# Kernel tuning notes

Measured on AMD Instinct MI355X. Metric: run time of the kernel, lower is better.

The kernel has to match this reference:

```python
import jax, jax.numpy as jnp
import numpy as np

B, C, H, W = 8, 320, 64, 64
NUM_SAMPLES = 3


def _skew(v):
    z = jnp.zeros((), v.dtype)
    return jnp.stack([
        jnp.stack([z, -v[2], v[1]]),
        jnp.stack([v[2], z, -v[0]]),
        jnp.stack([-v[1], v[0], z]),
    ])


def _rodrigues(rv):
    theta = jnp.linalg.norm(rv)
    r = rv / jnp.maximum(theta, 1e-12)
    I = jnp.eye(3, dtype=rv.dtype)
    R = jnp.cos(theta) * I + (1 - jnp.cos(theta)) * jnp.outer(r, r) + jnp.sin(theta) * _skew(r)
    return jnp.where(theta < 1e-6, I, R)


def _fundamental(Ks, Kt, ps, pt):
    Rs = jax.vmap(_rodrigues)(ps[:, :3])
    Rt = jax.vmap(_rodrigues)(pt[:, :3])
    ts, tt = ps[:, 3:], pt[:, 3:]
    R_rel = jnp.einsum('bij,bkj->bik', Rs, Rt)          # R_s @ R_t^T
    t_rel = ts - jnp.einsum('bij,bj->bi', R_rel, tt)
    E = jnp.einsum('bij,bjk->bik', jax.vmap(_skew)(t_rel), R_rel)
    inv_Ks = jnp.linalg.inv(Ks)
    inv_Kt = jnp.linalg.inv(Kt)
    return jnp.einsum('bji,bjk,bkl->bil', inv_Kt, E, inv_Ks)  # inv(Kt)^T @ E @ inv(Ks)


def _epipolar_warp(x, Ks, Kt, ps, pt, conv_w, conv_b):
    Bs, Cc, Hh, Ww = x.shape
    Fm = _fundamental(Ks, Kt, ps, pt)
    # pixel homogeneous coords, row-major flatten; H==W makes torch's i*H+j
    # loop index identical to this flat order
    k = jnp.arange(Hh * Ww)
    px = (k % Ww).astype(x.dtype)
    py = (k // Ww).astype(x.dtype)
    P = jnp.stack([px, py, jnp.ones_like(px)])            # [3, HW]
    lines = jnp.einsum('bji,jn->bin', Fm, P)              # F^T @ P -> [B,3,HW]
    a, b, c = lines[:, 0], lines[:, 1], lines[:, 2]
    W1, H1 = float(Ww - 1), float(Hh - 1)
    EPS = 1e-10
    x1 = jnp.clip(-c / (a + EPS), 0.0, W1)
    x2 = jnp.clip(-(b * H1 + c) / (a + EPS), 0.0, W1)
    y1 = jnp.clip(-c / (b + EPS), 0.0, H1)
    y2 = jnp.clip(-(a * W1 + c) / (b + EPS), 0.0, H1)
    t = jnp.linspace(0.0, 1.0, NUM_SAMPLES, dtype=x.dtype)
    sx = (x1[..., None] * (1 - t) + x2[..., None] * t).reshape(Bs, -1)  # [B, HW*3]
    sy = (y1[..., None] * (1 - t) + y2[..., None] * t).reshape(Bs, -1)
    # bilinear sampling; grid_sample(align_corners=True) normalization round-trips
    # back to pixel coords, and all samples are in-bounds by construction
    x0 = jnp.floor(sx)
    y0 = jnp.floor(sy)
    wx = sx - x0
    wy = sy - y0
    x0i = jnp.clip(x0, 0, Ww - 1).astype(jnp.int32)
    x1i = jnp.clip(x0 + 1, 0, Ww - 1).astype(jnp.int32)
    y0i = jnp.clip(y0, 0, Hh - 1).astype(jnp.int32)
    y1i = jnp.clip(y0 + 1, 0, Hh - 1).astype(jnp.int32)
    flat = x.reshape(Bs, Cc, Hh * Ww)

    def gather(yi, xi):
        return jnp.take_along_axis(flat, (yi * Ww + xi)[:, None, :], axis=2)  # [B,C,HW*3]

    g00, g10 = gather(y0i, x0i), gather(y0i, x1i)
    g01, g11 = gather(y1i, x0i), gather(y1i, x1i)
    wx_, wy_ = wx[:, None], wy[:, None]
    val = (g00 * (1 - wx_) * (1 - wy_) + g10 * wx_ * (1 - wy_)
           + g01 * (1 - wx_) * wy_ + g11 * wx_ * wy_)
    sampled = val.reshape(Bs, Cc, Hh * Ww, NUM_SAMPLES).mean(-1).reshape(Bs, Cc, Hh, Ww)
    out = jax.lax.conv_general_dilated(sampled, conv_w, (1, 1), 'SAME',
                                       dimension_numbers=('NCHW', 'OIHW', 'NCHW'))
    out = out + conv_b[None, :, None, None]
    return jax.nn.relu(out)


def setup_inputs() -> dict:
    key = jax.random.key(0)
    ks = jax.random.split(key, 8)
    x = jax.random.normal(ks[0], (B, C, H, W), dtype=jnp.float32)

    def make_K(kk):
        f = jax.random.uniform(kk, (B,), minval=400.0, maxval=600.0, dtype=jnp.float32)
        K = jnp.zeros((B, 3, 3), jnp.float32)
        K = K.at[:, 0, 0].set(f).at[:, 1, 1].set(f)
        K = K.at[:, 0, 2].set(W / 2.0).at[:, 1, 2].set(H / 2.0).at[:, 2, 2].set(1.0)
        return K

    source_intrinsics = make_K(ks[1])
    target_intrinsics = make_K(ks[2])
    source_pose = jnp.concatenate([
        0.3 * jax.random.normal(ks[3], (B, 3), jnp.float32),
        jax.random.normal(ks[4], (B, 3), jnp.float32)], axis=1)
    target_pose = jnp.concatenate([
        0.3 * jax.random.normal(ks[5], (B, 3), jnp.float32),
        jax.random.normal(ks[6], (B, 3), jnp.float32)], axis=1)
    fan_in = C * 3 * 3
    conv_w = jax.random.normal(ks[7], (C, C, 3, 3), jnp.float32) / np.sqrt(fan_in)
    conv_b = jnp.zeros((C,), jnp.float32)
    return {"x": x, "source_intrinsics": source_intrinsics,
            "target_intrinsics": target_intrinsics, "source_pose": source_pose,
            "target_pose": target_pose, "conv_w": conv_w, "conv_b": conv_b}


def reference(x, source_intrinsics, target_intrinsics, source_pose, target_pose, conv_w, conv_b):
    return _epipolar_warp(x, source_intrinsics, target_intrinsics,
                          source_pose, target_pose, conv_w, conv_b)
```

## Files before the change

### kernel.cpp

```cpp
#include <hip/hip_runtime.h>
#include <math.h>

#define BATCH 8
#define CH 320
#define HW 4096

typedef unsigned short u16;
typedef __attribute__((ext_vector_type(8))) short bf16x8;
typedef __attribute__((ext_vector_type(8))) unsigned short u16x8;
typedef __attribute__((ext_vector_type(4))) float f32x4;
typedef __attribute__((ext_vector_type(4))) float float4v;

#define ZP_OFF 0
#define SAMP_OFF 788480
#define WT_OFF 21760000

#define IBUF_BYTES 17408
#define A_OFF (2*IBUF_BYTES)
#define APHASE 61440
#define LDS_TOTAL (A_OFF + 2*APHASE)

__device__ __forceinline__ u16 f2bf(float f) {
    union { float f; unsigned u; } v; v.f = f;
    unsigned r = v.u + 0x7fffu + ((v.u >> 16) & 1u);
    return (u16)(r >> 16);
}
__device__ __forceinline__ float bf2f(u16 h) {
    union { unsigned u; float f; } v; v.u = ((unsigned)h) << 16;
    return v.f;
}
__device__ __forceinline__ void gl_lds16(const void* g, void* l) {
    __builtin_amdgcn_global_load_lds(
        (const __attribute__((address_space(1))) unsigned*)g,
        (__attribute__((address_space(3))) unsigned*)l, 16, 0, 0);
}

__device__ __forceinline__ void rodrigues3(float rv0, float rv1, float rv2, float* R) {
    float theta = sqrtf(rv0*rv0 + rv1*rv1 + rv2*rv2);
    float it = 1.0f / fmaxf(theta, 1e-12f);
    float r0 = rv0*it, r1 = rv1*it, r2 = rv2*it;
    float c = cosf(theta), s = sinf(theta), o = 1.0f - c;
    R[0]=c+o*r0*r0;    R[1]=o*r0*r1-s*r2; R[2]=o*r0*r2+s*r1;
    R[3]=o*r1*r0+s*r2; R[4]=c+o*r1*r1;    R[5]=o*r1*r2-s*r0;
    R[6]=o*r2*r0-s*r1; R[7]=o*r2*r1+s*r0; R[8]=c+o*r2*r2;
    if (theta < 1e-6f) { R[0]=1;R[1]=0;R[2]=0;R[3]=0;R[4]=1;R[5]=0;R[6]=0;R[7]=0;R[8]=1; }
}

__device__ __forceinline__ void inv3(const float* M, float* o) {
    float a=M[0],b=M[1],c=M[2],d=M[3],e=M[4],f=M[5],g=M[6],h=M[7],i=M[8];
    float A = e*i - f*h, B = f*g - d*i, C = d*h - e*g;
    float id = 1.0f / (a*A + b*B + c*C);
    o[0]=A*id;         o[1]=(c*h-b*i)*id; o[2]=(b*f-c*e)*id;
    o[3]=B*id;         o[4]=(a*i-c*g)*id; o[5]=(c*d-a*f)*id;
    o[6]=C*id;         o[7]=(b*g-a*h)*id; o[8]=(a*e-b*d)*id;
}

__device__ void compute_F(const float* Ks, const float* Kt, const float* ps,
                          const float* pt, int b, float* Fm) {
    float Rs[9], Rt[9];
    rodrigues3(ps[b*6+0], ps[b*6+1], ps[b*6+2], Rs);
    rodrigues3(pt[b*6+0], pt[b*6+1], pt[b*6+2], Rt);
    float Rr[9];
    #pragma unroll
    for (int i = 0; i < 3; ++i)
      #pragma unroll
      for (int k = 0; k < 3; ++k)
        Rr[i*3+k] = Rs[i*3+0]*Rt[k*3+0] + Rs[i*3+1]*Rt[k*3+1] + Rs[i*3+2]*Rt[k*3+2];
    float tt0 = pt[b*6+3], tt1 = pt[b*6+4], tt2 = pt[b*6+5];
    float tr0 = ps[b*6+3] - (Rr[0]*tt0 + Rr[1]*tt1 + Rr[2]*tt2);
    float tr1 = ps[b*6+4] - (Rr[3]*tt0 + Rr[4]*tt1 + Rr[5]*tt2);
    float tr2 = ps[b*6+5] - (Rr[6]*tt0 + Rr[7]*tt1 + Rr[8]*tt2);
    float E[9];
    #pragma unroll
    for (int j = 0; j < 3; ++j) {
        E[0*3+j] = -tr2*Rr[1*3+j] + tr1*Rr[2*3+j];
        E[1*3+j] =  tr2*Rr[0*3+j] - tr0*Rr[2*3+j];
        E[2*3+j] = -tr1*Rr[0*3+j] + tr0*Rr[1*3+j];
    }
    float iKs[9], iKt[9];
    inv3(Ks + b*9, iKs);
    inv3(Kt + b*9, iKt);
    float T[9];
    #pragma unroll
    for (int i = 0; i < 3; ++i)
      #pragma unroll
      for (int k = 0; k < 3; ++k)
        T[i*3+k] = iKt[0*3+i]*E[0*3+k] + iKt[1*3+i]*E[1*3+k] + iKt[2*3+i]*E[2*3+k];
    #pragma unroll
    for (int i = 0; i < 3; ++i)
      #pragma unroll
      for (int l = 0; l < 3; ++l)
        Fm[i*3 + l] = T[i*3+0]*iKs[0*3+l] + T[i*3+1]*iKs[1*3+l] + T[i*3+2]*iKs[2*3+l];
}

#define PLIDX(p) (((p)<<3) ^ (((p)&0x70)>>1))

__global__ __launch_bounds__(512) void k_sample8(const float* __restrict__ x,
                                                 const float* __restrict__ Ks,
                                                 const float* __restrict__ Kt,
                                                 const float* __restrict__ ps,
                                                 const float* __restrict__ pt,
                                                 const float* __restrict__ wsrc,
                                                 u16* __restrict__ wt,
                                                 float* __restrict__ zp,
                                                 u16* __restrict__ st) {
    __shared__ u16 pl[HW*8];
    int cg = blockIdx.x, b = blockIdx.y;
    int tid = threadIdx.x;
    int bid = b*40 + cg;

    for (int e = bid*512 + tid; e < 9*CH*CH; e += 320*512) {
        int cl = e & 31;
        int r  = e >> 5;
        int co = r % CH;
        int q  = r / CH;
        int t  = q % 9;
        int cc = q / 9;
        int ci = cc*32 + cl;
        wt[e] = f2bf(wsrc[((size_t)co*CH + ci)*9 + t]);
    }
    if (bid == 0 && tid < 256) zp[tid] = 0.0f;

    const float* xb = x + ((size_t)b*CH + cg*8)*HW;
    const float4v* xb4 = (const float4v*)xb;
    #pragma unroll
    for (int it = 0; it < 2; ++it) {
        int i0 = (it*512 + tid)*4;
        float4v v[8];
        #pragma unroll
        for (int c = 0; c < 8; ++c) v[c] = xb4[c*(HW/4) + it*512 + tid];
        #pragma unroll
        for (int j = 0; j < 4; ++j) {
            u16x8 o;
            #pragma unroll
            for (int c = 0; c < 8; ++c) o[c] = f2bf(v[c][j]);
            int pix = i0 + j;
            *(u16x8*)(pl + PLIDX(pix)) = o;
        }
    }
    float Fm[9];
    compute_F(Ks, Kt, ps, pt, b, Fm);
    __syncthreads();
    const float EPS = 1e-10f, W1 = 63.0f, H1 = 63.0f;
    for (int k = tid; k < HW; k += 512) {
        float px = (float)(k & 63);
        float py = (float)(k >> 6);
        float a  = Fm[0]*px + Fm[3]*py + Fm[6];
        float bb = Fm[1]*px + Fm[4]*py + Fm[7];
        float c  = Fm[2]*px + Fm[5]*py + Fm[8];
        float x1 = fminf(fmaxf(-c/(a+EPS), 0.0f), W1);
        float x2 = fminf(fmaxf(-(bb*H1+c)/(a+EPS), 0.0f), W1);
        float y1 = fminf(fmaxf(-c/(bb+EPS), 0.0f), H1);
        float y2 = fminf(fmaxf(-(a*W1+c)/(bb+EPS), 0.0f), H1);
        float sxs[3], sys[3];
        sxs[0] = x1; sys[0] = y1;
        sxs[1] = 0.5f*(x1+x2); sys[1] = 0.5f*(y1+y2);
        sxs[2] = x2; sys[2] = y2;
        float acc[8];
        #pragma unroll
        for (int c2 = 0; c2 < 8; ++c2) acc[c2] = 0.f;
        #pragma unroll
        for (int s = 0; s < 3; ++s) {
            float sx = sxs[s], sy = sys[s];
            float fx = floorf(sx), fy = floorf(sy);
            float wx = sx-fx, wy = sy-fy;
            int x0 = (int)fx, y0 = (int)fy;
            int x1i = min(x0+1,63), y1i = min(y0+1,63);
            u16x8 g00 = *(const u16x8*)(pl + PLIDX(y0*64+x0));
            u16x8 g10 = *(const u16x8*)(pl + PLIDX(y0*64+x1i));
            u16x8 g01 = *(const u16x8*)(pl + PLIDX(y1i*64+x0));
            u16x8 g11 = *(const u16x8*)(pl + PLIDX(y1i*64+x1i));
            float w00=(1.f-wx)*(1.f-wy), w10=wx*(1.f-wy), w01=(1.f-wx)*wy, w11=wx*wy;
            #pragma unroll
            for (int c2 = 0; c2 < 8; ++c2)
                acc[c2] += w00*bf2f(g00[c2]) + w10*bf2f(g10[c2])
                         + w01*bf2f(g01[c2]) + w11*bf2f(g11[c2]);
        }
        u16x8 o;
        #pragma unroll
        for (int c2 = 0; c2 < 8; ++c2) o[c2] = f2bf(acc[c2]*(1.f/3.f));
        *(u16x8*)(st + ((size_t)b*HW + k)*CH + cg*8) = o;
    }
}

__global__ __launch_bounds__(512, 1) void k_conv(const u16* __restrict__ st,
                                                 const u16* __restrict__ wt,
                                                 const float* __restrict__ bias,
                                                 const float* __restrict__ zp,
                                                 float* __restrict__ out) {
    __shared__ __align__(16) char lds[LDS_TOTAL];
    int rowblk = blockIdx.x;
    int b      = blockIdx.y;
    int y0 = rowblk*2;
    int lane = threadIdx.x & 63;
    int w = threadIdx.x >> 6;
    int wrow = w & 1;
    int co0w = (w >> 1) * 80;
    int l15 = lane & 15, l4 = lane >> 4;

    const u16* ga[3];
    int js[3];
    #pragma unroll
    for (int s = 0; s < 3; ++s) {
        int j = (s < 2) ? (s*8 + w) : 16;
        js[s] = j;
        int g = j*64 + lane;
        int row_l = g/264;
        int rem = g - row_l*264;
        int col = rem >> 2;
        int slot = rem & 3;
        int ks = slot ^ ((col>>1)&3);
        int yy = y0 - 1 + row_l;
        int xx = col - 1;
        bool oob = (g >= 1056) | (yy < 0) | (yy > 63) | (xx < 0) | (xx > 63);
        int yc = min(max(yy,0),63), xc = min(max(xx,0),63);
        const u16* p = st + (((size_t)b*HW) + yc*64 + xc)*CH + ks*8;
        ga[s] = oob ? (const u16*)zp : p;
    }
    int nslot = (w == 0) ? 3 : 2;

    int alaneoff = ((lane>>2)<<6) + ((((lane&3) ^ ((lane>>3)&3))) << 4);
    const char* asrc = (const char*)wt + alaneoff;

    int ard_off = (co0w + l15)*64 + ((l4 ^ ((l15>>1)&3)) << 4);

    f32x4 acc[5][4];
    #pragma unroll
    for (int mr = 0; mr < 5; ++mr)
        #pragma unroll
        for (int nf = 0; nf < 4; ++nf) acc[mr][nf] = (f32x4){0.f,0.f,0.f,0.f};

    #pragma unroll
    for (int s = 0; s < 3; ++s)
        if (s < nslot) gl_lds16(ga[s], lds + js[s]*1024);
    #pragma unroll
    for (int s = 0; s < 3; ++s) ga[s] += 32;
    #pragma unroll
    for (int s = 0; s < 8; ++s) {
        int j = s*8 + w;
        if (j < 60) gl_lds16(asrc + j*1024, lds + A_OFF + j*1024);
    }
    asrc += APHASE;
    __syncthreads();

    for (int c = 0; c < 10; ++c) {
        const char* ibuf = lds + (c&1)*IBUF_BYTES;
        #pragma unroll
        for (int ky = 0; ky < 3; ++ky) {
            int p = c*3 + ky;
            if (p < 29) {
                char* adst = lds + A_OFF + ((p+1)&1)*APHASE;
                #pragma unroll
                for (int s = 0; s < 8; ++s) {
                    int j = s*8 + w;
                    if (j < 60) gl_lds16(asrc + j*1024, adst + j*1024);
                }
                asrc += APHASE;
            }
            if (ky == 0 && c < 9) {
                char* idst = lds + ((c&1)^1)*IBUF_BYTES;
                #pragma unroll
                for (int s = 0; s < 3; ++s)
                    if (s < nslot) gl_lds16(ga[s], idst + js[s]*1024);
                #pragma unroll
                for (int s = 0; s < 3; ++s) ga[s] += 32;
            }
            const char* abuf = lds + A_OFF + (p&1)*APHASE;
            int rowbase = (wrow + ky) * 4224;
            #pragma unroll
            for (int kx = 0; kx < 3; ++kx) {
                bf16x8 bb[4];
                #pragma unroll
                for (int nf = 0; nf < 4; ++nf) {
                    int col = nf*16 + l15 + kx;
                    int boff = rowbase + col*64 + ((l4 ^ ((col>>1)&3))<<4);
                    bb[nf] = *(const bf16x8*)(ibuf + boff);
                }
                bf16x8 a[5];
                #pragma unroll
                for (int mr = 0; mr < 5; ++mr)
                    a[mr] = *(const bf16x8*)(abuf + kx*20480 + mr*1024 + ard_off);
                #pragma unroll
                for (int mr = 0; mr < 5; ++mr)
                    #pragma unroll
                    for (int nf = 0; nf < 4; ++nf)
                        acc[mr][nf] = __builtin_amdgcn_mfma_f32_16x16x32_bf16(
                            a[mr], bb[nf], acc[mr][nf], 0, 0, 0);
            }
            __syncthreads();
        }
    }

    int y = y0 + wrow;
    #pragma unroll
    for (int mr = 0; mr < 5; ++mr) {
        #pragma unroll
        for (int r = 0; r < 4; ++r) {
            int co = co0w + mr*16 + l4*4 + r;
            float bv = bias[co];
            float* ob = out + ((size_t)(b*CH + co))*HW + y*64;
            #pragma unroll
            for (int nf = 0; nf < 4; ++nf) {
                int xx = nf*16 + l15;
                ob[xx] = fmaxf(acc[mr][nf][r] + bv, 0.f);
            }
        }
    }
}

extern "C" void kernel_launch(void* const* d_in, const int* in_sizes, int n_in,
                              void* d_out, int out_size, void* d_ws, size_t ws_size,
                              hipStream_t stream) {
    const float* x  = (const float*)d_in[0];
    const float* Ks = (const float*)d_in[1];
    const float* Kt = (const float*)d_in[2];
    const float* ps = (const float*)d_in[3];
    const float* pt = (const float*)d_in[4];
    const float* cw = (const float*)d_in[5];
    const float* cb = (const float*)d_in[6];
    float* out = (float*)d_out;
    char* ws = (char*)d_ws;
    float* zp = (float*)(ws + ZP_OFF);
    u16*   st = (u16*)(ws + SAMP_OFF);
    u16*   wt = (u16*)(ws + WT_OFF);

    k_sample8<<<dim3(CH/8, BATCH), 512, 0, stream>>>(x, Ks, Kt, ps, pt, cw, wt, zp, st);
    k_conv<<<dim3(32, BATCH), 512, 0, stream>>>(st, wt, cb, zp, out);
}
```

Baseline: 88.72 us.

## Precompute per-pixel bilinear sample descriptors once per batch in a separate kernel

Epipolar line, sample-coordinate and bilinear-weight computation moves out of the per-channel-group sampling kernel into a new k_coords kernel. That kernel writes packed LDS offsets and bf16 weights per pixel and sample. The sampling kernel then only loads descriptors and gathers, so it no longer repeats the divisions and floors for each of the 40 channel groups. The cost is an extra kernel launch, a descriptor round-trip through global memory, and bf16 rounding of the interpolation weights, which slightly changes numerics.

```diff
diff --git a/kernel.cpp b/kernel.cpp
--- a/kernel.cpp
+++ b/kernel.cpp
@@ -14,6 +14,7 @@
 #define ZP_OFF 0
 #define SAMP_OFF 788480
 #define WT_OFF 21760000
+#define DESC_OFF 23603200
 
 #define IBUF_BYTES 17408
 #define A_OFF (2*IBUF_BYTES)
@@ -28,6 +29,9 @@
 __device__ __forceinline__ float bf2f(u16 h) {
     union { unsigned u; float f; } v; v.u = ((unsigned)h) << 16;
     return v.f;
+}
+__device__ __forceinline__ float bitf(unsigned u) {
+    union { unsigned u; float f; } v; v.u = u; return v.f;
 }
 __device__ __forceinline__ void gl_lds16(const void* g, void* l) {
     __builtin_amdgcn_global_load_lds(
@@ -95,21 +99,19 @@
 
 #define PLIDX(p) (((p)<<3) ^ (((p)&0x70)>>1))
 
-__global__ __launch_bounds__(512) void k_sample8(const float* __restrict__ x,
-                                                 const float* __restrict__ Ks,
-                                                 const float* __restrict__ Kt,
-                                                 const float* __restrict__ ps,
-                                                 const float* __restrict__ pt,
-                                                 const float* __restrict__ wsrc,
-                                                 u16* __restrict__ wt,
-                                                 float* __restrict__ zp,
-                                                 u16* __restrict__ st) {
-    __shared__ u16 pl[HW*8];
-    int cg = blockIdx.x, b = blockIdx.y;
-    int tid = threadIdx.x;
-    int bid = b*40 + cg;
-
-    for (int e = bid*512 + tid; e < 9*CH*CH; e += 320*512) {
+__global__ __launch_bounds__(512) void k_coords(const float* __restrict__ Ks,
+                                                const float* __restrict__ Kt,
+                                                const float* __restrict__ ps,
+                                                const float* __restrict__ pt,
+                                                const float* __restrict__ wsrc,
+                                                u16* __restrict__ wt,
+                                                float* __restrict__ zp,
+                                                uint4* __restrict__ desc) {
+    int b = blockIdx.y;
+    int k = blockIdx.x*512 + threadIdx.x;
+    int gid = (b*8 + blockIdx.x)*512 + threadIdx.x;
+
+    for (int e = gid; e < 9*CH*CH; e += 32768) {
         int cl = e & 31;
         int r  = e >> 5;
         int co = r % CH;
@@ -119,7 +121,51 @@
         int ci = cc*32 + cl;
         wt[e] = f2bf(wsrc[((size_t)co*CH + ci)*9 + t]);
     }
-    if (bid == 0 && tid < 256) zp[tid] = 0.0f;
+    if (gid < 256) zp[gid] = 0.0f;
+
+    float Fm[9];
+    compute_F(Ks, Kt, ps, pt, b, Fm);
+    const float EPS = 1e-10f, W1 = 63.0f, H1 = 63.0f;
+    float px = (float)(k & 63);
+    float py = (float)(k >> 6);
+    float a  = Fm[0]*px + Fm[3]*py + Fm[6];
+    float bb = Fm[1]*px + Fm[4]*py + Fm[7];
+    float c  = Fm[2]*px + Fm[5]*py + Fm[8];
+    float x1 = fminf(fmaxf(-c/(a+EPS), 0.0f), W1);
+    float x2 = fminf(fmaxf(-(bb*H1+c)/(a+EPS), 0.0f), W1);
+    float y1 = fminf(fmaxf(-c/(bb+EPS), 0.0f), H1);
+    float y2 = fminf(fmaxf(-(a*W1+c)/(bb+EPS), 0.0f), H1);
+    float sxs[3], sys[3];
+    sxs[0] = x1; sys[0] = y1;
+    sxs[1] = 0.5f*(x1+x2); sys[1] = 0.5f*(y1+y2);
+    sxs[2] = x2; sys[2] = y2;
+    #pragma unroll
+    for (int s = 0; s < 3; ++s) {
+        float sx = sxs[s], sy = sys[s];
+        float fx = floorf(sx), fy = floorf(sy);
+        float wx = sx-fx, wy = sy-fy;
+        int x0 = (int)fx, y0 = (int)fy;
+        int x1i = min(x0+1,63), y1i = min(y0+1,63);
+        unsigned o00 = (unsigned)PLIDX(y0*64+x0)  * 2u;
+        unsigned o10 = (unsigned)PLIDX(y0*64+x1i) * 2u;
+        unsigned o01 = (unsigned)PLIDX(y1i*64+x0) * 2u;
+        unsigned o11 = (unsigned)PLIDX(y1i*64+x1i)* 2u;
+        float w00=(1.f-wx)*(1.f-wy), w10=wx*(1.f-wy), w01=(1.f-wx)*wy, w11=wx*wy;
+        uint4 d;
+        d.x = o00 | (o10 << 16);
+        d.y = o01 | (o11 << 16);
+        d.z = (unsigned)f2bf(w00) | ((unsigned)f2bf(w10) << 16);
+        d.w = (unsigned)f2bf(w01) | ((unsigned)f2bf(w11) << 16);
+        desc[((size_t)b*3 + s)*HW + k] = d;
+    }
+}
+
+__global__ __launch_bounds__(512) void k_sample8(const float* __restrict__ x,
+                                                 const uint4* __restrict__ desc,
+                                                 u16* __restrict__ st) {
+    __shared__ u16 pl[HW*8];
+    int cg = blockIdx.x, b = blockIdx.y;
+    int tid = threadIdx.x;
 
     const float* xb = x + ((size_t)b*CH + cg*8)*HW;
     const float4v* xb4 = (const float4v*)xb;
@@ -138,39 +184,22 @@
             *(u16x8*)(pl + PLIDX(pix)) = o;
         }
     }
-    float Fm[9];
-    compute_F(Ks, Kt, ps, pt, b, Fm);
     __syncthreads();
-    const float EPS = 1e-10f, W1 = 63.0f, H1 = 63.0f;
+    const char* pb = (const char*)pl;
+    const uint4* db = desc + (size_t)b*3*HW;
     for (int k = tid; k < HW; k += 512) {
-        float px = (float)(k & 63);
-        float py = (float)(k >> 6);
-        float a  = Fm[0]*px + Fm[3]*py + Fm[6];
-        float bb = Fm[1]*px + Fm[4]*py + Fm[7];
-        float c  = Fm[2]*px + Fm[5]*py + Fm[8];
-        float x1 = fminf(fmaxf(-c/(a+EPS), 0.0f), W1);
-        float x2 = fminf(fmaxf(-(bb*H1+c)/(a+EPS), 0.0f), W1);
-        float y1 = fminf(fmaxf(-c/(bb+EPS), 0.0f), H1);
-        float y2 = fminf(fmaxf(-(a*W1+c)/(bb+EPS), 0.0f), H1);
-        float sxs[3], sys[3];
-        sxs[0] = x1; sys[0] = y1;
-        sxs[1] = 0.5f*(x1+x2); sys[1] = 0.5f*(y1+y2);
-        sxs[2] = x2; sys[2] = y2;
         float acc[8];
         #pragma unroll
         for (int c2 = 0; c2 < 8; ++c2) acc[c2] = 0.f;
         #pragma unroll
         for (int s = 0; s < 3; ++s) {
-            float sx = sxs[s], sy = sys[s];
-            float fx = floorf(sx), fy = floorf(sy);
-            float wx = sx-fx, wy = sy-fy;
-            int x0 = (int)fx, y0 = (int)fy;
-            int x1i = min(x0+1,63), y1i = min(y0+1,63);
-            u16x8 g00 = *(const u16x8*)(pl + PLIDX(y0*64+x0));
-            u16x8 g10 = *(const u16x8*)(pl + PLIDX(y0*64+x1i));
-            u16x8 g01 = *(const u16x8*)(pl + PLIDX(y1i*64+x0));
-            u16x8 g11 = *(const u16x8*)(pl + PLIDX(y1i*64+x1i));
-            float w00=(1.f-wx)*(1.f-wy), w10=wx*(1.f-wy), w01=(1.f-wx)*wy, w11=wx*wy;
+            uint4 d = db[s*HW + k];
+            u16x8 g00 = *(const u16x8*)(pb + (d.x & 0xffffu));
+            u16x8 g10 = *(const u16x8*)(pb + (d.x >> 16));
+            u16x8 g01 = *(const u16x8*)(pb + (d.y & 0xffffu));
+            u16x8 g11 = *(const u16x8*)(pb + (d.y >> 16));
+            float w00 = bitf(d.z << 16), w10 = bitf(d.z & 0xffff0000u);
+            float w01 = bitf(d.w << 16), w11 = bitf(d.w & 0xffff0000u);
             #pragma unroll
             for (int c2 = 0; c2 < 8; ++c2)
                 acc[c2] += w00*bf2f(g00[c2]) + w10*bf2f(g10[c2])
@@ -320,10 +349,12 @@
     const float* cb = (const float*)d_in[6];
     float* out = (float*)d_out;
     char* ws = (char*)d_ws;
-    float* zp = (float*)(ws + ZP_OFF);
-    u16*   st = (u16*)(ws + SAMP_OFF);
-    u16*   wt = (u16*)(ws + WT_OFF);
-
-    k_sample8<<<dim3(CH/8, BATCH), 512, 0, stream>>>(x, Ks, Kt, ps, pt, cw, wt, zp, st);
+    float* zp   = (float*)(ws + ZP_OFF);
+    u16*   st   = (u16*)(ws + SAMP_OFF);
+    u16*   wt   = (u16*)(ws + WT_OFF);
+    uint4* desc = (uint4*)(ws + DESC_OFF);
+
+    k_coords<<<dim3(HW/512, BATCH), 512, 0, stream>>>(Ks, Kt, ps, pt, cw, wt, zp, desc);
+    k_sample8<<<dim3(CH/8, BATCH), 512, 0, stream>>>(x, desc, st);
     k_conv<<<dim3(32, BATCH), 512, 0, stream>>>(st, wt, cb, zp, out);
 }
```

Result: slower. 95.77 us (+7.9%).
